# Optimization experiments

Hardware: AMD Instinct MI355X
Metric: run time of the kernel (lower is better)

The kernel has to match this reference:

```python
import jax, jax.numpy as jnp
from jax import lax
import numpy as np

B, T, F = 32, 8192, 16
HID = 128
OUT = 24
K1 = 10


def setup_inputs() -> dict:
    key = jax.random.key(0)
    ks = jax.random.split(key, 5)
    x = jax.random.normal(ks[0], (B, T, F), dtype=jnp.float32)
    # Conv1d(F -> HID, kernel=10): weight (O, I, K), bias (O,)
    w1 = jax.random.normal(ks[1], (HID, F, K1), dtype=jnp.float32) * (1.0 / np.sqrt(F * K1))
    b1 = jax.random.normal(ks[2], (HID,), dtype=jnp.float32) * 0.01
    # Linear(HID*10 -> OUT): weight (OUT, HID*10), bias (OUT,)
    wf = jax.random.normal(ks[3], (OUT, HID * K1), dtype=jnp.float32) * (1.0 / np.sqrt(HID * K1))
    bf = jax.random.normal(ks[4], (OUT,), dtype=jnp.float32) * 0.01
    return {"x": x, "w1": w1, "b1": b1, "wf": wf, "bf": bf}


def reference(x, w1, b1, wf, bf):
    # x: (B, T, F) -> (B, F, T)
    xc = jnp.transpose(x, (0, 2, 1))
    # Conv1d k=10, pad=9 -> length T+9
    h = lax.conv_general_dilated(
        xc, w1, window_strides=(1,), padding=[(9, 9)],
        dimension_numbers=("NCH", "OIH", "NCH")) + b1[None, :, None]  # (B, HID, T+9)
    # out[:, :x.shape[2], :] keeps the first T timesteps
    h = h[:, :, :x.shape[1]]
    h = jnp.concatenate([jnp.repeat(h[:, :, :1], 9, axis=2), h], axis=2)
    # Per-step Linear over flattened 10-step windows == valid conv with k=10.
    # flatten order of window (10, C) is time-major: col index = t*C + c
    kf = jnp.transpose(wf.reshape(wf.shape[0], K1, -1), (0, 2, 1))  # (OUT, HID, 10)
    y = lax.conv_general_dilated(
        h, kf, window_strides=(1,), padding="VALID",
        dimension_numbers=("NCH", "OIH", "NCH")) + bf[None, :, None]  # (B, OUT, T)
    return jnp.transpose(y, (0, 2, 1))  # (B, T, OUT)
```

## Files before the change

### kernel.cpp

```cpp
#include <hip/hip_runtime.h>

#define B_   32
#define T_   8192
#define F_   16
#define OUT_ 24
#define K1_  10
#define ND   19
#define NDP  20
#define JP   32
#define PADL 24
#define XROWS_TOT (PADL + T_ + 8)

#define WS_BC_OFF   20480
#define WS_E_OFF    20576
#define WS_W1T_OFF  144992
#define WS_XBF_OFF  226944

typedef short short8 __attribute__((ext_vector_type(8)));
typedef float float4v __attribute__((ext_vector_type(4)));

__device__ __forceinline__ unsigned short f2bf(float f) {
    unsigned u = __builtin_bit_cast(unsigned, f);
    unsigned r = (u + 0x7fffu + ((u >> 16) & 1u)) >> 16;
    return (unsigned short)r;
}

__device__ __forceinline__ short8 cvt8(float4 f0, float4 f1) {
    short8 v;
    v[0] = (short)f2bf(f0.x); v[1] = (short)f2bf(f0.y);
    v[2] = (short)f2bf(f0.z); v[3] = (short)f2bf(f0.w);
    v[4] = (short)f2bf(f1.x); v[5] = (short)f2bf(f1.y);
    v[6] = (short)f2bf(f1.z); v[7] = (short)f2bf(f1.w);
    return v;
}

__global__ void w1t_kernel(const float* __restrict__ w1, float* __restrict__ w1t) {
    int idx = blockIdx.x * 256 + threadIdx.x;
    float v = w1[idx];
    int c = idx / 160;
    int rem = idx - c * 160;
    int i = rem / 10;
    int k = rem - i * 10;
    w1t[(k * 16 + i) * 128 + c] = v;
}

__global__ __launch_bounds__(256) void xbf_kernel(const float* __restrict__ x,
                                                  unsigned short* __restrict__ xbf) {
    int id = blockIdx.x * 256 + threadIdx.x;
    if (id >= B_ * XROWS_TOT) return;
    int b = id / XROWS_TOT, r = id - b * XROWS_TOT;
    unsigned short* dst = xbf + (size_t)id * 16;
    int t = r - PADL;
    short8 v0 = short8{0,0,0,0,0,0,0,0}, v1 = v0;
    if (t >= 0 && t < T_) {
        const float4* p = (const float4*)(x + ((long)b * T_ + t) * 16);
        float4 f0 = p[0], f1 = p[1], f2 = p[2], f3 = p[3];
        v0 = cvt8(f0, f1);
        v1 = cvt8(f2, f3);
    }
    *(short8*)dst = v0;
    *(short8*)(dst + 8) = v1;
}

__global__ void prep_kernel(const float* __restrict__ w1t, const float* __restrict__ b1,
                            const float* __restrict__ wf, const float* __restrict__ bf,
                            unsigned short* __restrict__ w2pk, float* __restrict__ bcg,
                            float* __restrict__ Eg) {
    int blk = blockIdx.x;
    int c = threadIdx.x;
    __shared__ float red[16][128];
    __shared__ float red2[128];

    if (blk < JP * NDP) {
        int j = blk / NDP, d = blk % NDP;
        float p[16];
#pragma unroll
        for (int i = 0; i < 16; ++i) p[i] = 0.f;
        if (j < OUT_ && d < ND) {
            int klo = d - 9 > 0 ? d - 9 : 0;
            int khi = d < 9 ? d : 9;
            for (int k = klo; k <= khi; ++k) {
                float wfv = wf[j * 1280 + k * 128 + c];
                int k2 = d - k;
#pragma unroll
                for (int i = 0; i < 16; ++i)
                    p[i] = fmaf(wfv, w1t[(k2 * 16 + i) * 128 + c], p[i]);
            }
        }
#pragma unroll
        for (int i = 0; i < 16; ++i) red[i][c] = p[i];
        __syncthreads();
        for (int off = 64; off > 0; off >>= 1) {
            if (c < off) {
#pragma unroll
                for (int i = 0; i < 16; ++i) red[i][c] += red[i][c + off];
            }
            __syncthreads();
        }
        if (c < 16) {
            int kk = d * 16 + c;
            int ks = kk >> 5, r = kk & 31;
            int quad = r >> 3, z = r & 7;
            int tbl = j >> 4, jj = j & 15;
            int lane = jj + quad * 16;
            w2pk[((tbl * 10 + ks) * 64 + lane) * 8 + z] = f2bf(red[c][0]);
        }
        if (j < OUT_ && d == ND) {
            float s = 0.f;
#pragma unroll
            for (int k = 0; k < K1_; ++k) s += wf[j * 1280 + k * 128 + c];
            s *= b1[c];
            red2[c] = s;
            __syncthreads();
            for (int off = 64; off > 0; off >>= 1) {
                if (c < off) red2[c] += red2[c + off];
                __syncthreads();
            }
            if (c == 0) bcg[j] = bf[j] + red2[0];
        }
    } else {
        int eidx = blk - JP * NDP;
        int t = eidx / 216;
        int rem = eidx % 216;
        int j = rem / 9, tau = rem % 9;
        float p[16];
#pragma unroll
        for (int i = 0; i < 16; ++i) p[i] = 0.f;
        for (int k = 0; k < K1_; ++k) {
            int u = t + k - 9; if (u < 0) u = 0;
            if (tau > u) continue;
            int kap = tau + 9 - u;
#pragma unroll
            for (int i = 0; i < 16; ++i)
                p[i] = fmaf(wf[j * 1280 + k * 128 + c], w1t[(kap * 16 + i) * 128 + c], p[i]);
        }
#pragma unroll
        for (int i = 0; i < 16; ++i) red[i][c] = p[i];
        __syncthreads();
        for (int off = 64; off > 0; off >>= 1) {
            if (c < off) {
#pragma unroll
                for (int i = 0; i < 16; ++i) red[i][c] += red[i][c + off];
            }
            __syncthreads();
        }
        if (c < 16) Eg[((t * OUT_ + j) * 9 + tau) * 16 + c] = red[c][0];
    }
}

__global__ __launch_bounds__(256) void head_kernel(const float* __restrict__ x,
                                                   const float* __restrict__ Eg,
                                                   const float* __restrict__ bcg,
                                                   float* __restrict__ out) {
    int b = blockIdx.x, tid = threadIdx.x;
    if (tid >= 9 * OUT_) return;
    int t = tid / OUT_, j = tid % OUT_;
    const float4* xv = (const float4*)(x + (long)b * T_ * F_);
    const float4* ev = (const float4*)(Eg + (long)tid * 144);
    float ax = 0.f, ay = 0.f, az = 0.f, aw = 0.f;
#pragma unroll
    for (int q = 0; q < 36; ++q) {
        float4 e = ev[q];
        float4 v = xv[q];
        ax = fmaf(e.x, v.x, ax);
        ay = fmaf(e.y, v.y, ay);
        az = fmaf(e.z, v.z, az);
        aw = fmaf(e.w, v.w, aw);
    }
    out[((long)b * T_ + t) * OUT_ + j] = bcg[j] + ((ax + ay) + (az + aw));
}

__global__ __launch_bounds__(256) void main_kernel(const unsigned short* __restrict__ xbf,
                                                   const unsigned short* __restrict__ w2pk,
                                                   const float* __restrict__ bcg,
                                                   float* __restrict__ out) {
    int tid = threadIdx.x;
    int lane = tid & 63, w = tid >> 6;
    int b = blockIdx.y;
    int t0 = blockIdx.x * 256;

    int m = lane & 15, quad = lane >> 4;
    int ih = (quad & 1) * 8;
    int dq = quad >> 1;
    const unsigned short* xb = xbf + (size_t)b * XROWS_TOT * 16;
    int base = PADL + t0 + w * 64 + m + dq - 18;
    const unsigned short* pk0 = w2pk + lane * 8;
    const unsigned short* pk1 = w2pk + 5120 + lane * 8;

    float4v acc[4][2];
#pragma unroll
    for (int mt = 0; mt < 4; ++mt)
#pragma unroll
        for (int nt = 0; nt < 2; ++nt) acc[mt][nt] = float4v{0.f, 0.f, 0.f, 0.f};

#pragma unroll
    for (int ks = 0; ks < 10; ++ks) {
        short8 b0 = *(const short8*)(pk0 + ks * 512);
        short8 b1 = *(const short8*)(pk1 + ks * 512);
#pragma unroll
        for (int mt = 0; mt < 4; ++mt) {
            short8 a = *(const short8*)(xb + (size_t)(base + mt * 16 + 2 * ks) * 16 + ih);
            acc[mt][0] = __builtin_amdgcn_mfma_f32_16x16x32_bf16(a, b0, acc[mt][0], 0, 0, 0);
            acc[mt][1] = __builtin_amdgcn_mfma_f32_16x16x32_bf16(a, b1, acc[mt][1], 0, 0, 0);
        }
    }

    long outb = (long)b * T_;
    float bc0 = bcg[m];
    float bc1 = (m < 8) ? bcg[16 + m] : 0.f;
#pragma unroll
    for (int mt = 0; mt < 4; ++mt) {
        int trow = t0 + w * 64 + mt * 16 + quad * 4;
#pragma unroll
        for (int reg = 0; reg < 4; ++reg) {
            int t = trow + reg;
            float* o = out + (outb + t) * OUT_;
            o[m] = acc[mt][0][reg] + bc0;
            if (m < 8) o[16 + m] = acc[mt][1][reg] + bc1;
        }
    }
}

extern "C" void kernel_launch(void* const* d_in, const int* in_sizes, int n_in,
                              void* d_out, int out_size, void* d_ws, size_t ws_size,
                              hipStream_t stream) {
    const float* x  = (const float*)d_in[0];
    const float* w1 = (const float*)d_in[1];
    const float* b1 = (const float*)d_in[2];
    const float* wf = (const float*)d_in[3];
    const float* bf = (const float*)d_in[4];
    float* out = (float*)d_out;
    unsigned short* w2pk = (unsigned short*)d_ws;
    float* bcg = (float*)((char*)d_ws + WS_BC_OFF);
    float* Eg  = (float*)((char*)d_ws + WS_E_OFF);
    float* w1t = (float*)((char*)d_ws + WS_W1T_OFF);
    unsigned short* xbf = (unsigned short*)((char*)d_ws + WS_XBF_OFF);

    hipLaunchKernelGGL(w1t_kernel, dim3(80), dim3(256), 0, stream, w1, w1t);
    hipLaunchKernelGGL(xbf_kernel, dim3((B_ * XROWS_TOT + 255) / 256), dim3(256), 0, stream,
                       x, xbf);
    hipLaunchKernelGGL(prep_kernel, dim3(JP * NDP + 9 * OUT_ * 9), dim3(128), 0, stream,
                       w1t, b1, wf, bf, w2pk, bcg, Eg);
    hipLaunchKernelGGL(main_kernel, dim3(T_ / 256, B_), dim3(256), 0, stream,
                       xbf, w2pk, bcg, out);
    hipLaunchKernelGGL(head_kernel, dim3(B_), dim3(256), 0, stream,
                       x, Eg, bcg, out);
}
```

Measured before the change: 103.7 us.

## Fuse prep launches, use wave-level shuffle reductions, fold head into main kernel

The five launches become three. The xbf conversion, the w1 transpose and the zeroing of w2pk padding are merged into one pre_kernel, and the head computation runs as an extra block column inside main_kernel, which skips writing the first 9 rows at the edge to avoid a race. prep_kernel now gives each (j,d) task to one wave and reduces with shuffle-xor instead of LDS tree reductions with many barriers. main_kernel also preloads all B fragments into registers before the MFMA loop. The aim is to remove launch gaps and sync overhead in the prep stages, at the cost of more register pressure in main_kernel.

Result: no change. 102.7 us (-0.9%).

```diff
diff --git a/kernel.cpp b/kernel.cpp
--- a/kernel.cpp
+++ b/kernel.cpp
@@ -6,7 +6,6 @@
 #define OUT_ 24
 #define K1_  10
 #define ND   19
-#define NDP  20
 #define JP   32
 #define PADL 24
 #define XROWS_TOT (PADL + T_ + 8)
@@ -34,92 +33,107 @@
     return v;
 }
 
-__global__ void w1t_kernel(const float* __restrict__ w1, float* __restrict__ w1t) {
-    int idx = blockIdx.x * 256 + threadIdx.x;
-    float v = w1[idx];
-    int c = idx / 160;
-    int rem = idx - c * 160;
-    int i = rem / 10;
-    int k = rem - i * 10;
-    w1t[(k * 16 + i) * 128 + c] = v;
-}
-
-__global__ __launch_bounds__(256) void xbf_kernel(const float* __restrict__ x,
-                                                  unsigned short* __restrict__ xbf) {
-    int id = blockIdx.x * 256 + threadIdx.x;
-    if (id >= B_ * XROWS_TOT) return;
-    int b = id / XROWS_TOT, r = id - b * XROWS_TOT;
-    unsigned short* dst = xbf + (size_t)id * 16;
-    int t = r - PADL;
-    short8 v0 = short8{0,0,0,0,0,0,0,0}, v1 = v0;
-    if (t >= 0 && t < T_) {
-        const float4* p = (const float4*)(x + ((long)b * T_ + t) * 16);
-        float4 f0 = p[0], f1 = p[1], f2 = p[2], f3 = p[3];
-        v0 = cvt8(f0, f1);
-        v1 = cvt8(f2, f3);
-    }
-    *(short8*)dst = v0;
-    *(short8*)(dst + 8) = v1;
-}
-
-__global__ void prep_kernel(const float* __restrict__ w1t, const float* __restrict__ b1,
-                            const float* __restrict__ wf, const float* __restrict__ bf,
-                            unsigned short* __restrict__ w2pk, float* __restrict__ bcg,
-                            float* __restrict__ Eg) {
-    int blk = blockIdx.x;
-    int c = threadIdx.x;
-    __shared__ float red[16][128];
-    __shared__ float red2[128];
-
-    if (blk < JP * NDP) {
-        int j = blk / NDP, d = blk % NDP;
+__global__ __launch_bounds__(256) void pre_kernel(const float* __restrict__ x,
+                                                  const float* __restrict__ w1,
+                                                  unsigned short* __restrict__ xbf,
+                                                  float* __restrict__ w1t,
+                                                  unsigned short* __restrict__ w2pk) {
+    int bx = blockIdx.x;
+    int tid = threadIdx.x;
+    if (bx < 1028) {
+        int id = bx * 256 + tid;
+        if (id >= B_ * XROWS_TOT) return;
+        int b = id / XROWS_TOT, r = id - b * XROWS_TOT;
+        unsigned short* dst = xbf + (size_t)id * 16;
+        int t = r - PADL;
+        short8 v0 = short8{0,0,0,0,0,0,0,0}, v1 = v0;
+        if (t >= 0 && t < T_) {
+            const float4* p = (const float4*)(x + ((long)b * T_ + t) * 16);
+            float4 f0 = p[0], f1 = p[1], f2 = p[2], f3 = p[3];
+            v0 = cvt8(f0, f1);
+            v1 = cvt8(f2, f3);
+        }
+        *(short8*)dst = v0;
+        *(short8*)(dst + 8) = v1;
+    } else if (bx < 1108) {
+        int idx = (bx - 1028) * 256 + tid;
+        float v = w1[idx];
+        int c = idx / 160;
+        int rem = idx - c * 160;
+        int i = rem / 10;
+        int k = rem - i * 10;
+        w1t[(k * 16 + i) * 128 + c] = v;
+    } else {
+        int idx = (bx - 1108) * 256 + tid;
+        ((unsigned*)w2pk)[idx] = 0;
+    }
+}
+
+__global__ __launch_bounds__(256) void prep_kernel(const float* __restrict__ w1t,
+                                                   const float* __restrict__ b1,
+                                                   const float* __restrict__ wf,
+                                                   const float* __restrict__ bf,
+                                                   unsigned short* __restrict__ w2pk,
+                                                   float* __restrict__ bcg,
+                                                   float* __restrict__ Eg) {
+    int tid = threadIdx.x;
+    int lane = tid & 63;
+    int wid = blockIdx.x * 4 + (tid >> 6);
+
+    if (wid < 456) {
+        int j = wid / ND, d = wid % ND;
         float p[16];
 #pragma unroll
         for (int i = 0; i < 16; ++i) p[i] = 0.f;
-        if (j < OUT_ && d < ND) {
-            int klo = d - 9 > 0 ? d - 9 : 0;
-            int khi = d < 9 ? d : 9;
-            for (int k = klo; k <= khi; ++k) {
-                float wfv = wf[j * 1280 + k * 128 + c];
-                int k2 = d - k;
-#pragma unroll
-                for (int i = 0; i < 16; ++i)
-                    p[i] = fmaf(wfv, w1t[(k2 * 16 + i) * 128 + c], p[i]);
-            }
-        }
-#pragma unroll
-        for (int i = 0; i < 16; ++i) red[i][c] = p[i];
-        __syncthreads();
-        for (int off = 64; off > 0; off >>= 1) {
-            if (c < off) {
-#pragma unroll
-                for (int i = 0; i < 16; ++i) red[i][c] += red[i][c + off];
-            }
-            __syncthreads();
-        }
-        if (c < 16) {
-            int kk = d * 16 + c;
+        int klo = d - 9 > 0 ? d - 9 : 0;
+        int khi = d < 9 ? d : 9;
+        for (int k = klo; k <= khi; ++k) {
+            float w0 = wf[j * 1280 + k * 128 + lane];
+            float w1v = wf[j * 1280 + k * 128 + 64 + lane];
+            const float* wb = w1t + (d - k) * 16 * 128;
+#pragma unroll
+            for (int i = 0; i < 16; ++i)
+                p[i] = fmaf(w0, wb[i * 128 + lane], fmaf(w1v, wb[i * 128 + 64 + lane], p[i]));
+        }
+#pragma unroll
+        for (int i = 0; i < 16; ++i) {
+            p[i] += __shfl_xor(p[i], 1);
+            p[i] += __shfl_xor(p[i], 2);
+            p[i] += __shfl_xor(p[i], 4);
+            p[i] += __shfl_xor(p[i], 8);
+            p[i] += __shfl_xor(p[i], 16);
+            p[i] += __shfl_xor(p[i], 32);
+        }
+        if (lane < 16) {
+            float v = p[0];
+#pragma unroll
+            for (int i = 1; i < 16; ++i)
+                if (lane == i) v = p[i];
+            int kk = d * 16 + lane;
             int ks = kk >> 5, r = kk & 31;
             int quad = r >> 3, z = r & 7;
             int tbl = j >> 4, jj = j & 15;
-            int lane = jj + quad * 16;
-            w2pk[((tbl * 10 + ks) * 64 + lane) * 8 + z] = f2bf(red[c][0]);
-        }
-        if (j < OUT_ && d == ND) {
-            float s = 0.f;
-#pragma unroll
-            for (int k = 0; k < K1_; ++k) s += wf[j * 1280 + k * 128 + c];
-            s *= b1[c];
-            red2[c] = s;
-            __syncthreads();
-            for (int off = 64; off > 0; off >>= 1) {
-                if (c < off) red2[c] += red2[c + off];
-                __syncthreads();
-            }
-            if (c == 0) bcg[j] = bf[j] + red2[0];
-        }
+            int lt = jj + quad * 16;
+            w2pk[((tbl * 10 + ks) * 64 + lt) * 8 + z] = f2bf(v);
+        }
+    } else if (wid < 480) {
+        int j = wid - 456;
+        float s0 = 0.f, s1 = 0.f;
+#pragma unroll
+        for (int k = 0; k < K1_; ++k) {
+            s0 += wf[j * 1280 + k * 128 + lane];
+            s1 += wf[j * 1280 + k * 128 + 64 + lane];
+        }
+        float s = s0 * b1[lane] + s1 * b1[64 + lane];
+        s += __shfl_xor(s, 1);
+        s += __shfl_xor(s, 2);
+        s += __shfl_xor(s, 4);
+        s += __shfl_xor(s, 8);
+        s += __shfl_xor(s, 16);
+        s += __shfl_xor(s, 32);
+        if (lane == 0) bcg[j] = bf[j] + s;
     } else {
-        int eidx = blk - JP * NDP;
+        int eidx = wid - 480;
         int t = eidx / 216;
         int rem = eidx % 216;
         int j = rem / 9, tau = rem % 9;
@@ -130,53 +144,61 @@
             int u = t + k - 9; if (u < 0) u = 0;
             if (tau > u) continue;
             int kap = tau + 9 - u;
+            float w0 = wf[j * 1280 + k * 128 + lane];
+            float w1v = wf[j * 1280 + k * 128 + 64 + lane];
+            const float* wb = w1t + kap * 16 * 128;
 #pragma unroll
             for (int i = 0; i < 16; ++i)
-                p[i] = fmaf(wf[j * 1280 + k * 128 + c], w1t[(kap * 16 + i) * 128 + c], p[i]);
-        }
-#pragma unroll
-        for (int i = 0; i < 16; ++i) red[i][c] = p[i];
-        __syncthreads();
-        for (int off = 64; off > 0; off >>= 1) {
-            if (c < off) {
-#pragma unroll
-                for (int i = 0; i < 16; ++i) red[i][c] += red[i][c + off];
-            }
-            __syncthreads();
-        }
-        if (c < 16) Eg[((t * OUT_ + j) * 9 + tau) * 16 + c] = red[c][0];
-    }
-}
-
-__global__ __launch_bounds__(256) void head_kernel(const float* __restrict__ x,
-                                                   const float* __restrict__ Eg,
-                                                   const float* __restrict__ bcg,
-                                                   float* __restrict__ out) {
-    int b = blockIdx.x, tid = threadIdx.x;
-    if (tid >= 9 * OUT_) return;
-    int t = tid / OUT_, j = tid % OUT_;
-    const float4* xv = (const float4*)(x + (long)b * T_ * F_);
-    const float4* ev = (const float4*)(Eg + (long)tid * 144);
-    float ax = 0.f, ay = 0.f, az = 0.f, aw = 0.f;
-#pragma unroll
-    for (int q = 0; q < 36; ++q) {
-        float4 e = ev[q];
-        float4 v = xv[q];
-        ax = fmaf(e.x, v.x, ax);
-        ay = fmaf(e.y, v.y, ay);
-        az = fmaf(e.z, v.z, az);
-        aw = fmaf(e.w, v.w, aw);
-    }
-    out[((long)b * T_ + t) * OUT_ + j] = bcg[j] + ((ax + ay) + (az + aw));
+                p[i] = fmaf(w0, wb[i * 128 + lane], fmaf(w1v, wb[i * 128 + 64 + lane], p[i]));
+        }
+#pragma unroll
+        for (int i = 0; i < 16; ++i) {
+            p[i] += __shfl_xor(p[i], 1);
+            p[i] += __shfl_xor(p[i], 2);
+            p[i] += __shfl_xor(p[i], 4);
+            p[i] += __shfl_xor(p[i], 8);
+            p[i] += __shfl_xor(p[i], 16);
+            p[i] += __shfl_xor(p[i], 32);
+        }
+        if (lane < 16) {
+            float v = p[0];
+#pragma unroll
+            for (int i = 1; i < 16; ++i)
+                if (lane == i) v = p[i];
+            Eg[((t * OUT_ + j) * 9 + tau) * 16 + lane] = v;
+        }
+    }
 }
 
 __global__ __launch_bounds__(256) void main_kernel(const unsigned short* __restrict__ xbf,
                                                    const unsigned short* __restrict__ w2pk,
                                                    const float* __restrict__ bcg,
-                                                   float* __restrict__ out) {
+                                                   float* __restrict__ out,
+                                                   const float* __restrict__ x,
+                                                   const float* __restrict__ Eg) {
     int tid = threadIdx.x;
+    int b = blockIdx.y;
+
+    if (blockIdx.x == 32) {
+        if (tid >= 9 * OUT_) return;
+        int t = tid / OUT_, j = tid % OUT_;
+        const float4* xv = (const float4*)(x + (long)b * T_ * F_);
+        const float4* ev = (const float4*)(Eg + (long)tid * 144);
+        float ax = 0.f, ay = 0.f, az = 0.f, aw = 0.f;
+#pragma unroll
+        for (int q = 0; q < 36; ++q) {
+            float4 e = ev[q];
+            float4 v = xv[q];
+            ax = fmaf(e.x, v.x, ax);
+            ay = fmaf(e.y, v.y, ay);
+            az = fmaf(e.z, v.z, az);
+            aw = fmaf(e.w, v.w, aw);
+        }
+        out[((long)b * T_ + t) * OUT_ + j] = bcg[j] + ((ax + ay) + (az + aw));
+        return;
+    }
+
     int lane = tid & 63, w = tid >> 6;
-    int b = blockIdx.y;
     int t0 = blockIdx.x * 256;
 
     int m = lane & 15, quad = lane >> 4;
@@ -187,6 +209,13 @@
     const unsigned short* pk0 = w2pk + lane * 8;
     const unsigned short* pk1 = w2pk + 5120 + lane * 8;
 
+    short8 B0[10], B1[10];
+#pragma unroll
+    for (int ks = 0; ks < 10; ++ks) {
+        B0[ks] = *(const short8*)(pk0 + ks * 512);
+        B1[ks] = *(const short8*)(pk1 + ks * 512);
+    }
+
     float4v acc[4][2];
 #pragma unroll
     for (int mt = 0; mt < 4; ++mt)
@@ -195,28 +224,29 @@
 
 #pragma unroll
     for (int ks = 0; ks < 10; ++ks) {
-        short8 b0 = *(const short8*)(pk0 + ks * 512);
-        short8 b1 = *(const short8*)(pk1 + ks * 512);
 #pragma unroll
         for (int mt = 0; mt < 4; ++mt) {
             short8 a = *(const short8*)(xb + (size_t)(base + mt * 16 + 2 * ks) * 16 + ih);
-            acc[mt][0] = __builtin_amdgcn_mfma_f32_16x16x32_bf16(a, b0, acc[mt][0], 0, 0, 0);
-            acc[mt][1] = __builtin_amdgcn_mfma_f32_16x16x32_bf16(a, b1, acc[mt][1], 0, 0, 0);
+            acc[mt][0] = __builtin_amdgcn_mfma_f32_16x16x32_bf16(a, B0[ks], acc[mt][0], 0, 0, 0);
+            acc[mt][1] = __builtin_amdgcn_mfma_f32_16x16x32_bf16(a, B1[ks], acc[mt][1], 0, 0, 0);
         }
     }
 
     long outb = (long)b * T_;
     float bc0 = bcg[m];
     float bc1 = (m < 8) ? bcg[16 + m] : 0.f;
+    bool edge = (blockIdx.x == 0);
 #pragma unroll
     for (int mt = 0; mt < 4; ++mt) {
         int trow = t0 + w * 64 + mt * 16 + quad * 4;
 #pragma unroll
         for (int reg = 0; reg < 4; ++reg) {
             int t = trow + reg;
-            float* o = out + (outb + t) * OUT_;
-            o[m] = acc[mt][0][reg] + bc0;
-            if (m < 8) o[16 + m] = acc[mt][1][reg] + bc1;
+            if (!edge || t >= 9) {
+                float* o = out + (outb + t) * OUT_;
+                o[m] = acc[mt][0][reg] + bc0;
+                if (m < 8) o[16 + m] = acc[mt][1][reg] + bc1;
+            }
         }
     }
 }
@@ -236,13 +266,10 @@
     float* w1t = (float*)((char*)d_ws + WS_W1T_OFF);
     unsigned short* xbf = (unsigned short*)((char*)d_ws + WS_XBF_OFF);
 
-    hipLaunchKernelGGL(w1t_kernel, dim3(80), dim3(256), 0, stream, w1, w1t);
-    hipLaunchKernelGGL(xbf_kernel, dim3((B_ * XROWS_TOT + 255) / 256), dim3(256), 0, stream,
-                       x, xbf);
-    hipLaunchKernelGGL(prep_kernel, dim3(JP * NDP + 9 * OUT_ * 9), dim3(128), 0, stream,
+    hipLaunchKernelGGL(pre_kernel, dim3(1148), dim3(256), 0, stream,
+                       x, w1, xbf, w1t, w2pk);
+    hipLaunchKernelGGL(prep_kernel, dim3(606), dim3(256), 0, stream,
                        w1t, b1, wf, bf, w2pk, bcg, Eg);
-    hipLaunchKernelGGL(main_kernel, dim3(T_ / 256, B_), dim3(256), 0, stream,
-                       xbf, w2pk, bcg, out);
-    hipLaunchKernelGGL(head_kernel, dim3(B_), dim3(256), 0, stream,
-                       x, Eg, bcg, out);
-}
+    hipLaunchKernelGGL(main_kernel, dim3(33, B_), dim3(256), 0, stream,
+                       xbf, w2pk, bcg, out, x, Eg);
+}
```
